# Performance work log

Measured on AMD Instinct MI355X. Metric: run time of the kernel, lower is better.

The kernel has to match this reference:

```python
import jax, jax.numpy as jnp
import numpy as np

NUM_VECTORS = 1024
LATENT_DIM = 256
BETA = 0.25


def setup_inputs() -> dict:
    key = jax.random.key(0)
    k1, k2 = jax.random.split(key)
    x = jax.random.normal(k1, (32, LATENT_DIM, 64, 64), dtype=jnp.float32)
    # torch init: uniform(-1/num_vectors, 1/num_vectors)
    emb = jax.random.uniform(k2, (NUM_VECTORS, LATENT_DIM), dtype=jnp.float32,
                             minval=-1.0 / NUM_VECTORS, maxval=1.0 / NUM_VECTORS)
    return {"x": x, "emb": emb}


def reference(x, emb):
    B, C, H, W = x.shape
    x_bhwc = jnp.transpose(x, (0, 2, 3, 1))          # [B,H,W,C]
    xf = x_bhwc.reshape(-1, C)                       # [N,C], N = B*H*W
    d = (jnp.sum(xf * xf, axis=1, keepdims=True)
         + jnp.sum(emb * emb, axis=1)
         - 2.0 * (xf @ emb.T))
    idx = jnp.argmin(d, axis=1)                      # [N]
    x_q = emb[idx].reshape(B, H, W, C)               # gather + reshape
    sg = jax.lax.stop_gradient
    loss = (jnp.mean((sg(x_q) - x_bhwc) ** 2)
            + BETA * jnp.mean((x_q - sg(x_bhwc)) ** 2))
    # straight-through estimator
    x_q_st = x_bhwc + sg(x_q - x_bhwc)
    x_q_out = jnp.transpose(x_q_st, (0, 3, 1, 2))    # [B,C,H,W]
    return (x_q_out, idx, loss)
```

## Files before the change

kernel.cpp:

```cpp
#include <hip/hip_runtime.h>
#include <cfloat>

#define NV    1024
#define CDIM  256
#define NROWS 131072
#define TOTAL 33554432
#define HW    4096
#define WWIN  3.5e-4f
#define MST   68
#define EST   261

typedef __attribute__((ext_vector_type(8))) short bf16x8;
typedef __attribute__((ext_vector_type(4))) float f32x4;

template <typename GET>
__device__ __forceinline__ float np_s128(const GET& get, int base) {
    float tv[16];
#pragma unroll
    for (int l = 0; l < 16; ++l) {
        float s0 = __fadd_rn(get(base + l),      get(base + 64 + l));
        float s1 = __fadd_rn(get(base + 16 + l), get(base + 80 + l));
        float s2 = __fadd_rn(get(base + 32 + l), get(base + 96 + l));
        float s3 = __fadd_rn(get(base + 48 + l), get(base + 112 + l));
        tv[l] = __fadd_rn(__fadd_rn(s0, s1), __fadd_rn(s2, s3));
    }
    float u[8];
#pragma unroll
    for (int l = 0; l < 8; ++l) u[l] = __fadd_rn(tv[l], tv[l + 8]);
    float v[4];
#pragma unroll
    for (int l = 0; l < 4; ++l) v[l] = __fadd_rn(u[l], u[l + 4]);
    return __fadd_rn(__fadd_rn(v[0], v[2]), __fadd_rn(v[1], v[3]));
}
template <typename GET>
__device__ __forceinline__ float np_s256(const GET& get) {
    return __fadd_rn(np_s128(get, 0), np_s128(get, 128));
}

__device__ __forceinline__ unsigned short f2bf_rne(float f) {
    unsigned u = __float_as_uint(f);
    unsigned r = u + 0x7fffu + ((u >> 16) & 1u);
    return (unsigned short)(r >> 16);
}

__device__ __forceinline__ float exact_d(const float* __restrict__ xrow,
                                         const float* __restrict__ erow,
                                         float sxn, float se) {
    float g = 0.f;
    for (int c = 0; c < CDIM; ++c) g = __fmaf_rn(xrow[c], erow[c], g);
    return __fsub_rn(__fadd_rn(sxn, se), __fmul_rn(2.0f, g));
}

__device__ __forceinline__ void gload_lds16(const void* gsrc, void* ldst) {
    __builtin_amdgcn_global_load_lds(
        (const __attribute__((address_space(1))) void*)gsrc,
        (__attribute__((address_space(3))) void*)ldst, 16, 0, 0);
}

__global__ __launch_bounds__(256) void prep_kernel(
        const float* __restrict__ emb, unsigned short* __restrict__ ehg,
        float* __restrict__ enf, double* loss, int* fbcnt) {
    __shared__ float sq[CDIM];
    const int k = blockIdx.x, c = threadIdx.x;
    if (k == 0 && c == 0) { *loss = 0.0; *fbcnt = 0; }
    const float e = emb[(size_t)k * CDIM + c];
    ehg[(size_t)k * CDIM + c] = f2bf_rne(e);
    sq[c] = __fmul_rn(e, e);
    __syncthreads();
    if (c == 0) {
        auto get = [](int i) { return ((const float*)sq)[i]; };
        enf[k] = np_s256(get);
    }
}

__global__ __launch_bounds__(256, 2) void gemm_argmin_kernel(
        const float* __restrict__ x, const float* __restrict__ emb,
        const unsigned short* __restrict__ ehg,
        const float* __restrict__ enf, int* __restrict__ idx,
        int* __restrict__ fb_list, int* __restrict__ fb_cnt) {
    __shared__ __align__(16) char sbuf[32768];

    const int tid  = threadIdx.x;
    const int lane = tid & 63;
    const int lcol = lane & 15;
    const int quad = lane >> 4;
    const int wid  = tid >> 6;
    const int wy   = wid >> 1;
    const int wx   = wid & 1;
    const int mbase = wy * 32;
    const int nl   = wx * 16 + lcol;

    const int rowbase = blockIdx.x * 64;
    const int b   = rowbase >> 12;
    const int hw0 = rowbase & 4095;
    const float* xb = x + ((size_t)b * CDIM) * HW + hw0;

    auto STAGE = [&](int buf, int ch) {
        char* dB = sbuf + (buf << 14);
        const int k0 = ch * 32;
#pragma unroll
        for (int it = 0; it < 4; ++it) {
            const int g  = it * 256 + tid;
            const int n  = g >> 5, p = g & 31;
            const int s5 = (p - n) & 31;
            const size_t src = (size_t)(k0 + n) * 256 + s5 * 8;
            gload_lds16(ehg + src, dB + g * 16);
        }
    };

    STAGE(0, 0);

    bf16x8 ah[2][8];
#pragma unroll
    for (int t = 0; t < 2; ++t) {
        const int m = mbase + t * 16 + lcol;
#pragma unroll
        for (int kc = 0; kc < 8; ++kc) {
            const int c0 = kc * 32 + quad * 8;
            float fv[8];
#pragma unroll
            for (int j = 0; j < 8; ++j) fv[j] = xb[(size_t)(c0 + j) * HW + m];
#pragma unroll
            for (int j = 0; j < 8; ++j) ah[t][kc][j] = (short)f2bf_rne(fv[j]);
        }
    }

    float m1[8], m2[8];
#pragma unroll
    for (int s = 0; s < 8; ++s) { m1[s] = FLT_MAX; m2[s] = FLT_MAX; }
    unsigned i1p[2] = { 0xffffffffu, 0xffffffffu };

    __syncthreads();

    int cur = 0;
    for (int ch = 0; ch < 32; ++ch) {
        if (ch < 31) STAGE(cur ^ 1, ch + 1);

        const unsigned short* sBh = (const unsigned short*)(sbuf + (cur << 14));

        const float enfv = enf[ch * 32 + nl];
        f32x4 acc[2];
        acc[0] = (f32x4){0.f, 0.f, 0.f, 0.f};
        acc[1] = (f32x4){0.f, 0.f, 0.f, 0.f};

#pragma unroll
        for (int kc = 0; kc < 8; ++kc) {
            const int s5  = kc * 4 + quad;
            const int off = nl * 256 + (((s5 + nl) & 31) * 8);
            const bf16x8 bh = *(const bf16x8*)&sBh[off];
#pragma unroll
            for (int t = 0; t < 2; ++t)
                acc[t] = __builtin_amdgcn_mfma_f32_16x16x32_bf16(
                    ah[t][kc], bh, acc[t], 0, 0, 0);
        }

#pragma unroll
        for (int t = 0; t < 2; ++t)
#pragma unroll
            for (int r = 0; r < 4; ++r) {
                const float z = __fmaf_rn(-2.0f, acc[t][r], enfv);
                const int s  = t * 4 + r;
                const int sh = r * 8;
                const bool lt1 = z < m1[s];
                m2[s] = __builtin_amdgcn_fmed3f(z, m1[s], m2[s]);
                m1[s] = fminf(z, m1[s]);
                const unsigned cand = (i1p[t] & ~(0xffu << sh)) | ((unsigned)ch << sh);
                i1p[t] = lt1 ? cand : i1p[t];
            }

        __syncthreads();
        cur ^= 1;
    }

    float* Mv1 = (float*)sbuf;
    int*   Mi1 = (int*)(sbuf + 8704);
    float* Mv2 = (float*)(sbuf + 17408);
#pragma unroll
    for (int t = 0; t < 2; ++t) {
        const int row0 = mbase + t * 16 + quad * 4;
        const int base = nl * MST + row0;
        *(float4*)&Mv1[base] = *(const float4*)&m1[t * 4];
        *(float4*)&Mv2[base] = *(const float4*)&m2[t * 4];
        int4 kk;
        kk.x = (int)((i1p[t] >>  0) & 0xffu) * 32 + nl;
        kk.y = (int)((i1p[t] >>  8) & 0xffu) * 32 + nl;
        kk.z = (int)((i1p[t] >> 16) & 0xffu) * 32 + nl;
        kk.w = (int)((i1p[t] >> 24) & 0xffu) * 32 + nl;
        *(int4*)&Mi1[base] = kk;
    }
    __syncthreads();

    if (tid < 64) {
        const int row = tid;
        float M = FLT_MAX;
#pragma unroll
        for (int c = 0; c < 32; ++c) M = fminf(M, Mv1[c * MST + row]);
        const float lim = M + WWIN;

        int cand[12]; int cnt = 0; bool overflow = false;
        for (int c = 0; c < 32; ++c) {
            if (Mv2[c * MST + row] <= lim) overflow = true;
            if (Mv1[c * MST + row] <= lim) {
                if (cnt < 12) cand[cnt++] = Mi1[c * MST + row] & (NV - 1);
                else overflow = true;
            }
        }
        if (overflow) {
            const int pos = atomicAdd(fb_cnt, 1);
            fb_list[pos] = rowbase + row;
        } else if (cnt == 1) {
            idx[rowbase + row] = cand[0];
        } else {
            auto g2 = [xb, row](int c) {
                const float v = xb[(size_t)c * HW + row];
                return __fmul_rn(v, v);
            };
            const float sxn = np_s256(g2);
            float bd = FLT_MAX; int bk = 0x7fffffff;
            for (int cc = 0; cc < cnt; ++cc) {
                const int kk = cand[cc];
                const float* er = emb + (size_t)kk * CDIM;
                float gacc = 0.f;
                for (int c2 = 0; c2 < CDIM; ++c2)
                    gacc = __fmaf_rn(xb[(size_t)c2 * HW + row], er[c2], gacc);
                const float d = __fsub_rn(__fadd_rn(sxn, enf[kk]),
                                          __fmul_rn(2.0f, gacc));
                if (d < bd || (d == bd && kk < bk)) { bd = d; bk = kk; }
            }
            idx[rowbase + row] = bk;
        }
    }
}

__global__ __launch_bounds__(256) void fallback_kernel(
        const float* __restrict__ x, const float* __restrict__ emb,
        const float* __restrict__ enf, int* __restrict__ idx,
        const int* __restrict__ fb_list, const int* __restrict__ fb_cnt) {
    __shared__ float sxr[CDIM];
    __shared__ float rv[256];
    __shared__ int   rk[256];

    const int n = *fb_cnt;
    for (int i = blockIdx.x; i < n; i += gridDim.x) {
        const int r  = fb_list[i];
        const int b  = r >> 12;
        const int hw = r & 4095;
        sxr[threadIdx.x] = x[((size_t)(b * CDIM + threadIdx.x)) * HW + hw];
        __syncthreads();

        auto get = [](int c) { float v = ((const float*)sxr)[c]; return __fmul_rn(v, v); };
        float sxn = np_s256(get);

        float bd = FLT_MAX; int bk = 0x7fffffff;
#pragma unroll
        for (int j = 0; j < 4; ++j) {
            const int k = threadIdx.x * 4 + j;
            float d = exact_d(sxr, emb + (size_t)k * CDIM, sxn, enf[k]);
            if (d < bd) { bd = d; bk = k; }
        }
        rv[threadIdx.x] = bd; rk[threadIdx.x] = bk;
        __syncthreads();
        for (int sft = 128; sft > 0; sft >>= 1) {
            if (threadIdx.x < sft) {
                float ov = rv[threadIdx.x + sft]; int ok = rk[threadIdx.x + sft];
                if (ov < rv[threadIdx.x] ||
                    (ov == rv[threadIdx.x] && ok < rk[threadIdx.x])) {
                    rv[threadIdx.x] = ov; rk[threadIdx.x] = ok;
                }
            }
            __syncthreads();
        }
        if (threadIdx.x == 0) idx[r] = rk[0];
        __syncthreads();
    }
}

__global__ __launch_bounds__(256) void gather_kernel(
        const float* __restrict__ x, const float* __restrict__ emb,
        const int* __restrict__ idx, float* __restrict__ out,
        float* __restrict__ oidx, double* __restrict__ loss) {
    __shared__ float sE[64][EST];
    __shared__ int   sidx[64];
    __shared__ double red[256];

    const int tid = threadIdx.x;
    const int rowbase = blockIdx.x * 64;
    const int b   = rowbase >> 12;
    const int hw0 = rowbase & 4095;

    if (tid < 64) sidx[tid] = idx[rowbase + tid];
    __syncthreads();

    if (tid < 64) oidx[rowbase + tid] = (float)sidx[tid];

    {
        const int r  = tid >> 2;
        const int qt = tid & 3;
        const float* e = emb + (size_t)sidx[r] * CDIM + qt * 64;
        for (int u = 0; u < 16; ++u) {
            float4 v = *(const float4*)(e + u * 4);
            *(float4*)&sE[r][qt * 64 + u * 4] = v;
        }
    }
    __syncthreads();

    const float* xb = x + ((size_t)b * CDIM) * HW + hw0;
    float* ob = out + ((size_t)b * CDIM) * HW + hw0;
    double s = 0.0;
    for (int it = 0; it < 16; ++it) {
        int c  = it * 16 + (tid >> 4);
        int m4 = (tid & 15) * 4;
        float4 ev;
        ev.x = sE[m4 + 0][c]; ev.y = sE[m4 + 1][c];
        ev.z = sE[m4 + 2][c]; ev.w = sE[m4 + 3][c];
        float4 xv = *(const float4*)(xb + (size_t)c * HW + m4);
        *(float4*)(ob + (size_t)c * HW + m4) = ev;
        float d0 = ev.x - xv.x, d1 = ev.y - xv.y, d2 = ev.z - xv.z, d3 = ev.w - xv.w;
        s = fma((double)d0, (double)d0, s);
        s = fma((double)d1, (double)d1, s);
        s = fma((double)d2, (double)d2, s);
        s = fma((double)d3, (double)d3, s);
    }
    red[tid] = s;
    __syncthreads();
    for (int sft = 128; sft > 0; sft >>= 1) {
        if (tid < sft) red[tid] += red[tid + sft];
        __syncthreads();
    }
    if (tid == 0) atomicAdd(loss, red[0]);
}

__global__ void fin_kernel(const double* __restrict__ loss, float* __restrict__ o) {
    *o = (float)(1.25 * (*loss) / (double)TOTAL);
}

extern "C" void kernel_launch(void* const* d_in, const int* in_sizes, int n_in,
                              void* d_out, int out_size, void* d_ws, size_t ws_size,
                              hipStream_t stream) {
    const float* x   = (const float*)d_in[0];
    const float* emb = (const float*)d_in[1];
    float* out = (float*)d_out;
    char*  ws  = (char*)d_ws;

    double* loss    = (double*)ws;
    int*    fb_cnt  = (int*)(ws + 8);
    float*  enf     = (float*)(ws + 64);
    int*    idx     = (int*)(ws + 64 + 4096);
    int*    fb_list = idx + NROWS;

    unsigned short* ehg = (unsigned short*)d_out;

    float* out_xq   = out;
    float* out_idx  = out + (size_t)TOTAL;
    float* out_loss = out + (size_t)TOTAL + NROWS;

    hipLaunchKernelGGL(prep_kernel,      dim3(NV),           dim3(256), 0, stream,
                       emb, ehg, enf, loss, fb_cnt);
    hipLaunchKernelGGL(gemm_argmin_kernel, dim3(NROWS / 64), dim3(256), 0, stream,
                       x, emb, ehg, enf, idx, fb_list, fb_cnt);
    hipLaunchKernelGGL(fallback_kernel,  dim3(256),          dim3(256), 0, stream,
                       x, emb, enf, idx, fb_list, fb_cnt);
    hipLaunchKernelGGL(gather_kernel,    dim3(NROWS / 64),   dim3(256), 0, stream,
                       x, emb, idx, out_xq, out_idx, loss);
    hipLaunchKernelGGL(fin_kernel,       dim3(1),            dim3(1),   0, stream, loss, out_loss);
}
```

Baseline: 445.5 us.

## Fuse codebook gather and loss into GEMM-argmin kernel, drop separate gather pass

The separate gather kernel is removed. The GEMM/argmin kernel now stages the selected codebook rows in enlarged shared memory, writes the quantized output and float indices, and accumulates the squared-error loss, with overflow rows masked out. The fallback kernel now writes its rows' outputs and loss contributions directly. This avoids a second full pass over x, the idx round trip and one kernel launch, at the cost of more LDS per block and a longer GEMM-kernel epilogue.

```diff
diff --git a/kernel.cpp b/kernel.cpp
--- a/kernel.cpp
+++ b/kernel.cpp
@@ -76,9 +76,11 @@
 __global__ __launch_bounds__(256, 2) void gemm_argmin_kernel(
         const float* __restrict__ x, const float* __restrict__ emb,
         const unsigned short* __restrict__ ehg,
-        const float* __restrict__ enf, int* __restrict__ idx,
+        const float* __restrict__ enf,
+        float* __restrict__ out, float* __restrict__ oidx,
+        double* __restrict__ loss,
         int* __restrict__ fb_list, int* __restrict__ fb_cnt) {
-    __shared__ __align__(16) char sbuf[32768];
+    __shared__ __align__(16) char smem[69376];
 
     const int tid  = threadIdx.x;
     const int lane = tid & 63;
@@ -96,7 +98,7 @@
     const float* xb = x + ((size_t)b * CDIM) * HW + hw0;
 
     auto STAGE = [&](int buf, int ch) {
-        char* dB = sbuf + (buf << 14);
+        char* dB = smem + (buf << 14);
         const int k0 = ch * 32;
 #pragma unroll
         for (int it = 0; it < 4; ++it) {
@@ -136,7 +138,7 @@
     for (int ch = 0; ch < 32; ++ch) {
         if (ch < 31) STAGE(cur ^ 1, ch + 1);
 
-        const unsigned short* sBh = (const unsigned short*)(sbuf + (cur << 14));
+        const unsigned short* sBh = (const unsigned short*)(smem + (cur << 14));
 
         const float enfv = enf[ch * 32 + nl];
         f32x4 acc[2];
@@ -172,9 +174,12 @@
         cur ^= 1;
     }
 
-    float* Mv1 = (float*)sbuf;
-    int*   Mi1 = (int*)(sbuf + 8704);
-    float* Mv2 = (float*)(sbuf + 17408);
+    float* Mv1 = (float*)smem;
+    int*   Mi1 = (int*)(smem + 8704);
+    float* Mv2 = (float*)(smem + 17408);
+    int*   sidx = (int*)(smem + 66816);
+    int*   sovf = (int*)(smem + 67072);
+    double* red = (double*)(smem + 67328);
 #pragma unroll
     for (int t = 0; t < 2; ++t) {
         const int row0 = mbase + t * 16 + quad * 4;
@@ -205,11 +210,13 @@
                 else overflow = true;
             }
         }
+        int chosen;
         if (overflow) {
             const int pos = atomicAdd(fb_cnt, 1);
             fb_list[pos] = rowbase + row;
+            chosen = cand[0];
         } else if (cnt == 1) {
-            idx[rowbase + row] = cand[0];
+            chosen = cand[0];
         } else {
             auto g2 = [xb, row](int c) {
                 const float v = xb[(size_t)c * HW + row];
@@ -227,18 +234,68 @@
                                           __fmul_rn(2.0f, gacc));
                 if (d < bd || (d == bd && kk < bk)) { bd = d; bk = kk; }
             }
-            idx[rowbase + row] = bk;
-        }
-    }
+            chosen = bk;
+        }
+        sidx[row] = chosen;
+        sovf[row] = overflow ? 1 : 0;
+        if (!overflow) oidx[rowbase + row] = (float)chosen;
+    }
+    __syncthreads();
+
+    float* sE = (float*)smem;
+    {
+        const int r  = tid >> 2;
+        const int qt = tid & 3;
+        const float* e = emb + (size_t)sidx[r] * CDIM + qt * 64;
+        for (int u = 0; u < 16; ++u) {
+            float4 v = *(const float4*)(e + u * 4);
+            *(float4*)&sE[(size_t)r * EST + qt * 64 + u * 4] = v;
+        }
+    }
+    __syncthreads();
+
+    float* ob = out + ((size_t)b * CDIM) * HW + hw0;
+    const int m4 = (tid & 15) * 4;
+    const double w0 = sovf[m4 + 0] ? 0.0 : 1.0;
+    const double w1 = sovf[m4 + 1] ? 0.0 : 1.0;
+    const double w2 = sovf[m4 + 2] ? 0.0 : 1.0;
+    const double w3 = sovf[m4 + 3] ? 0.0 : 1.0;
+    double s = 0.0;
+    for (int it = 0; it < 16; ++it) {
+        const int c = it * 16 + (tid >> 4);
+        float4 ev;
+        ev.x = sE[(size_t)(m4 + 0) * EST + c];
+        ev.y = sE[(size_t)(m4 + 1) * EST + c];
+        ev.z = sE[(size_t)(m4 + 2) * EST + c];
+        ev.w = sE[(size_t)(m4 + 3) * EST + c];
+        float4 xv = *(const float4*)(xb + (size_t)c * HW + m4);
+        *(float4*)(ob + (size_t)c * HW + m4) = ev;
+        const double d0 = (double)(ev.x - xv.x), d1 = (double)(ev.y - xv.y);
+        const double d2 = (double)(ev.z - xv.z), d3 = (double)(ev.w - xv.w);
+        s = fma(w0 * d0, d0, s);
+        s = fma(w1 * d1, d1, s);
+        s = fma(w2 * d2, d2, s);
+        s = fma(w3 * d3, d3, s);
+    }
+    red[tid] = s;
+    __syncthreads();
+    for (int sft = 128; sft > 0; sft >>= 1) {
+        if (tid < sft) red[tid] += red[tid + sft];
+        __syncthreads();
+    }
+    if (tid == 0) atomicAdd(loss, red[0]);
 }
 
 __global__ __launch_bounds__(256) void fallback_kernel(
         const float* __restrict__ x, const float* __restrict__ emb,
-        const float* __restrict__ enf, int* __restrict__ idx,
+        const float* __restrict__ enf,
+        float* __restrict__ out, float* __restrict__ oidx,
+        double* __restrict__ loss,
         const int* __restrict__ fb_list, const int* __restrict__ fb_cnt) {
     __shared__ float sxr[CDIM];
     __shared__ float rv[256];
     __shared__ int   rk[256];
+    __shared__ double dred[256];
 
     const int n = *fb_cnt;
     for (int i = blockIdx.x; i < n; i += gridDim.x) {
@@ -270,64 +327,21 @@
             }
             __syncthreads();
         }
-        if (threadIdx.x == 0) idx[r] = rk[0];
-        __syncthreads();
-    }
-}
-
-__global__ __launch_bounds__(256) void gather_kernel(
-        const float* __restrict__ x, const float* __restrict__ emb,
-        const int* __restrict__ idx, float* __restrict__ out,
-        float* __restrict__ oidx, double* __restrict__ loss) {
-    __shared__ float sE[64][EST];
-    __shared__ int   sidx[64];
-    __shared__ double red[256];
-
-    const int tid = threadIdx.x;
-    const int rowbase = blockIdx.x * 64;
-    const int b   = rowbase >> 12;
-    const int hw0 = rowbase & 4095;
-
-    if (tid < 64) sidx[tid] = idx[rowbase + tid];
-    __syncthreads();
-
-    if (tid < 64) oidx[rowbase + tid] = (float)sidx[tid];
-
-    {
-        const int r  = tid >> 2;
-        const int qt = tid & 3;
-        const float* e = emb + (size_t)sidx[r] * CDIM + qt * 64;
-        for (int u = 0; u < 16; ++u) {
-            float4 v = *(const float4*)(e + u * 4);
-            *(float4*)&sE[r][qt * 64 + u * 4] = v;
-        }
-    }
-    __syncthreads();
-
-    const float* xb = x + ((size_t)b * CDIM) * HW + hw0;
-    float* ob = out + ((size_t)b * CDIM) * HW + hw0;
-    double s = 0.0;
-    for (int it = 0; it < 16; ++it) {
-        int c  = it * 16 + (tid >> 4);
-        int m4 = (tid & 15) * 4;
-        float4 ev;
-        ev.x = sE[m4 + 0][c]; ev.y = sE[m4 + 1][c];
-        ev.z = sE[m4 + 2][c]; ev.w = sE[m4 + 3][c];
-        float4 xv = *(const float4*)(xb + (size_t)c * HW + m4);
-        *(float4*)(ob + (size_t)c * HW + m4) = ev;
-        float d0 = ev.x - xv.x, d1 = ev.y - xv.y, d2 = ev.z - xv.z, d3 = ev.w - xv.w;
-        s = fma((double)d0, (double)d0, s);
-        s = fma((double)d1, (double)d1, s);
-        s = fma((double)d2, (double)d2, s);
-        s = fma((double)d3, (double)d3, s);
-    }
-    red[tid] = s;
-    __syncthreads();
-    for (int sft = 128; sft > 0; sft >>= 1) {
-        if (tid < sft) red[tid] += red[tid + sft];
-        __syncthreads();
-    }
-    if (tid == 0) atomicAdd(loss, red[0]);
+        const int kbest = rk[0];
+        const int c = threadIdx.x;
+        const float e = emb[(size_t)kbest * CDIM + c];
+        out[((size_t)(b * CDIM + c)) * HW + hw] = e;
+        if (c == 0) oidx[r] = (float)kbest;
+        const double d = (double)(e - sxr[c]);
+        dred[c] = d * d;
+        __syncthreads();
+        for (int sft = 128; sft > 0; sft >>= 1) {
+            if (c < sft) dred[c] += dred[c + sft];
+            __syncthreads();
+        }
+        if (c == 0) atomicAdd(loss, dred[0]);
+        __syncthreads();
+    }
 }
 
 __global__ void fin_kernel(const double* __restrict__ loss, float* __restrict__ o) {
@@ -345,10 +359,9 @@
     double* loss    = (double*)ws;
     int*    fb_cnt  = (int*)(ws + 8);
     float*  enf     = (float*)(ws + 64);
-    int*    idx     = (int*)(ws + 64 + 4096);
-    int*    fb_list = idx + NROWS;
-
-    unsigned short* ehg = (unsigned short*)d_out;
+    int*    fb_list = (int*)(ws + 64 + 4096);
+
+    unsigned short* ehg = (unsigned short*)(ws + 64 + 4096 + 4 * NROWS);
 
     float* out_xq   = out;
     float* out_idx  = out + (size_t)TOTAL;
@@ -357,10 +370,8 @@
     hipLaunchKernelGGL(prep_kernel,      dim3(NV),           dim3(256), 0, stream,
                        emb, ehg, enf, loss, fb_cnt);
     hipLaunchKernelGGL(gemm_argmin_kernel, dim3(NROWS / 64), dim3(256), 0, stream,
-                       x, emb, ehg, enf, idx, fb_list, fb_cnt);
+                       x, emb, ehg, enf, out_xq, out_idx, loss, fb_list, fb_cnt);
     hipLaunchKernelGGL(fallback_kernel,  dim3(256),          dim3(256), 0, stream,
-                       x, emb, enf, idx, fb_list, fb_cnt);
-    hipLaunchKernelGGL(gather_kernel,    dim3(NROWS / 64),   dim3(256), 0, stream,
-                       x, emb, idx, out_xq, out_idx, loss);
+                       x, emb, enf, out_xq, out_idx, loss, fb_list, fb_cnt);
     hipLaunchKernelGGL(fin_kernel,       dim3(1),            dim3(1),   0, stream, loss, out_loss);
 }
```

Result: slower. 503.3 us (+13.0%).
